# Kernel optimization log

Hardware: AMD Instinct MI355X
Metric: run time of the kernel (lower is better)

Reference implementation:

```python
import jax, jax.numpy as jnp
import numpy as np

N, E, IN, H, C, ED = 50000, 800000, 128, 4, 64, 4
NEG_SLOPE = 0.2


def setup_inputs() -> dict:
    key = jax.random.key(0)
    ks = iter(jax.random.split(key, 40))
    def p(shape, s=0.05):
        return jax.random.normal(next(ks), shape, jnp.float32) * s
    inp = dict(
        x=jax.random.normal(next(ks), (N, IN), jnp.float32),
        edge_index=jax.random.randint(next(ks), (2, E), 0, N),
        edge_attr=jax.random.normal(next(ks), (E, ED), jnp.float32),
        # GATConv layer 1 (concat=True)
        W1=p((IN, H * C)), att_src1=p((H, C)), att_dst1=p((H, C)),
        We1=p((ED, H * C)), att_e1=p((H, C)), b1=p((H * C,)),
        g1=jnp.ones((H * C,), jnp.float32), be1=jnp.zeros((H * C,), jnp.float32),
        # GATConv layer 2 (concat=False -> mean over heads)
        W2=p((H * C, H * C)), att_src2=p((H, C)), att_dst2=p((H, C)),
        We2=p((ED, H * C)), att_e2=p((H, C)), b2=p((C,)),
        g2=jnp.ones((C,), jnp.float32), be2=jnp.zeros((C,), jnp.float32),
        # skip / MLP head
        skip_W=p((IN, C)), skip_b=p((C,)),
        fc1_W=p((C, C // 2)), fc1_b=p((C // 2,)),
        fc2_W=p((C // 2, 1)), fc2_b=p((1,)),
    )
    return inp


def _add_self_loops(edge_index, edge_attr, n):
    # PyG GATConv default: add_self_loops=True, fill_value='mean'
    src, dst = edge_index[0], edge_index[1]
    sums = jax.ops.segment_sum(edge_attr, dst, num_segments=n)
    cnt = jax.ops.segment_sum(jnp.ones((edge_attr.shape[0], 1), edge_attr.dtype), dst, num_segments=n)
    mean_attr = sums / jnp.maximum(cnt, 1.0)
    loop = jnp.arange(n)
    src = jnp.concatenate([src, loop])
    dst = jnp.concatenate([dst, loop])
    ea = jnp.concatenate([edge_attr, mean_attr], axis=0)
    return src, dst, ea


def _gat_layer(x, src, dst, ea, W, a_src, a_dst, We, a_e, bias, n, concat):
    xs = (x @ W).reshape(n, H, C)                     # [N,H,C]
    alpha_src = (xs * a_src).sum(-1)                  # [N,H]
    alpha_dst = (xs * a_dst).sum(-1)                  # [N,H]
    ep = (ea @ We).reshape(-1, H, C)                  # [Et,H,C]
    alpha_e = (ep * a_e).sum(-1)                      # [Et,H]
    alpha = jax.nn.leaky_relu(alpha_src[src] + alpha_dst[dst] + alpha_e, NEG_SLOPE)
    # segment softmax over destination nodes
    m = jax.ops.segment_max(alpha, dst, num_segments=n)
    alpha = jnp.exp(alpha - m[dst])
    denom = jax.ops.segment_sum(alpha, dst, num_segments=n)
    alpha = alpha / (denom[dst] + 1e-16)
    out = jax.ops.segment_sum(xs[src] * alpha[:, :, None], dst, num_segments=n)  # [N,H,C]
    out = out.reshape(n, H * C) if concat else out.mean(axis=1)
    return out + bias


def _bn(x, g, b):
    mu = x.mean(0)
    var = x.var(0)
    return (x - mu) * jax.lax.rsqrt(var + 1e-5) * g + b


def reference(x, edge_index, edge_attr, W1, att_src1, att_dst1, We1, att_e1, b1, g1, be1,
              W2, att_src2, att_dst2, We2, att_e2, b2, g2, be2,
              skip_W, skip_b, fc1_W, fc1_b, fc2_W, fc2_b):
    n = x.shape[0]
    src, dst, ea = _add_self_loops(edge_index, edge_attr, n)
    residual = x @ skip_W + skip_b
    h = _gat_layer(x, src, dst, ea, W1, att_src1, att_dst1, We1, att_e1, b1, n, True)
    h = jax.nn.elu(_bn(h, g1, be1))
    h = _gat_layer(h, src, dst, ea, W2, att_src2, att_dst2, We2, att_e2, b2, n, False)
    h = jax.nn.elu(_bn(h, g2, be2))
    h = h + residual
    h = jax.nn.relu(h @ fc1_W + fc1_b)
    h = jax.nn.softplus(h @ fc2_W + fc2_b)
    return h.squeeze(-1)
```

## Files before the change

### kernel.cpp

```cpp
#include <hip/hip_runtime.h>
#include <math.h>

static constexpr int N_NODES = 50000;
static constexpr int N_EDGES = 800000;
static constexpr int IN_F = 128;
static constexpr int CH = 64;
static constexpr int HC = 256;
static constexpr float NEG_SLOPE = 0.2f;

typedef __attribute__((ext_vector_type(8))) short bf16x8;
typedef __attribute__((ext_vector_type(4))) float f32x4;

__device__ __forceinline__ unsigned pack_bf(float a, float b) {
    unsigned ua = __float_as_uint(a) + 0x8000u;
    unsigned ub = __float_as_uint(b) + 0x8000u;
    return __builtin_amdgcn_perm(ub, ua, 0x07060302u);
}
__device__ __forceinline__ float bflo(unsigned u) { return __uint_as_float(u << 16); }
__device__ __forceinline__ float bfhi(unsigned u) { return __uint_as_float(u & 0xffff0000u); }
__device__ __forceinline__ float bfs(unsigned short u) {
    return __uint_as_float((unsigned)u << 16);
}
__device__ __forceinline__ float elu(float v) { return v > 0.f ? v : __expf(v) - 1.0f; }

__device__ __forceinline__ int sigma(int p) { return ((p & 15) << 4) | (p >> 4); }

static constexpr int EB_BLK = (N_EDGES + 255) / 256;
static constexpr int CONV_ITEMS = 106496 + 32;
static constexpr int CONV_BLK = (CONV_ITEMS + 255) / 256;

__global__ void hist_conv(const int* __restrict__ ei, int* __restrict__ deg,
                          const float* __restrict__ W1, const float* __restrict__ W2,
                          const float* __restrict__ Ws, const float* __restrict__ We1,
                          const float* __restrict__ atte1, const float* __restrict__ We2,
                          const float* __restrict__ atte2, unsigned short* __restrict__ WT1,
                          unsigned short* __restrict__ WT2, unsigned short* __restrict__ WTs,
                          float* __restrict__ weff) {
    if (blockIdx.x < EB_BLK) {
        int e = blockIdx.x * 256 + threadIdx.x;
        if (e < N_EDGES) atomicAdd(&deg[ei[N_EDGES + e]], 1);
        return;
    }
    int t = (blockIdx.x - EB_BLK) * 256 + threadIdx.x;
    if (t < 32768) {
        int k = t >> 8, n = t & 255;
        unsigned u = __float_as_uint(W1[t]) + 0x8000u;
        WT1[n * 128 + k] = (unsigned short)(u >> 16);
    } else if (t < 98304) {
        int u2 = t - 32768;
        int k = u2 >> 8, n = u2 & 255;
        unsigned u = __float_as_uint(W2[u2]) + 0x8000u;
        WT2[n * 256 + sigma(k)] = (unsigned short)(u >> 16);
    } else if (t < 106496) {
        int u2 = t - 98304;
        int k = u2 >> 6, n = u2 & 63;
        unsigned u = __float_as_uint(Ws[u2]) + 0x8000u;
        WTs[n * 128 + k] = (unsigned short)(u >> 16);
    } else if (t < 106496 + 32) {
        int idx = t - 106496;
        const float* We = idx < 16 ? We1 : We2;
        const float* ae = idx < 16 ? atte1 : atte2;
        int j = idx & 15;
        int d = j >> 2, h = j & 3;
        float s = 0.f;
        for (int c = 0; c < CH; ++c) s += We[d * HC + h * CH + c] * ae[h * CH + c];
        weff[idx] = s;
    }
}

__global__ void scan_block(const int* __restrict__ deg, int* __restrict__ rowptr,
                           int* __restrict__ bsum) {
    __shared__ int s[256];
    int tid = threadIdx.x;
    int i = blockIdx.x * 256 + tid;
    int v = (i < N_NODES) ? deg[i] : 0;
    s[tid] = v;
    __syncthreads();
    for (int off = 1; off < 256; off <<= 1) {
        int t = (tid >= off) ? s[tid - off] : 0;
        __syncthreads();
        s[tid] += t;
        __syncthreads();
    }
    if (i < N_NODES) rowptr[i] = s[tid] - v;
    if (tid == 255) bsum[blockIdx.x] = s[255];
}

__global__ void scan_add2(int* __restrict__ rowptr, const int* __restrict__ bsum,
                          int* __restrict__ fillc, int nb) {
    __shared__ int s[256];
    int tid = threadIdx.x;
    int v = (tid < nb) ? bsum[tid] : 0;
    s[tid] = v;
    __syncthreads();
    for (int off = 1; off < 256; off <<= 1) {
        int t = (tid >= off) ? s[tid - off] : 0;
        __syncthreads();
        s[tid] += t;
        __syncthreads();
    }
    int boff = (blockIdx.x == 0) ? 0 : s[blockIdx.x - 1];
    int i = blockIdx.x * 256 + tid;
    if (i < N_NODES) {
        rowptr[i] += boff;
        fillc[i] = 0;
    }
    if (i == N_NODES) rowptr[N_NODES] = N_EDGES;
}

__global__ void csr_fill(const int* __restrict__ ei, const int* __restrict__ rowptr,
                         int* __restrict__ fillc, int* __restrict__ csr_src,
                         int* __restrict__ pos) {
    int e = blockIdx.x * blockDim.x + threadIdx.x;
    if (e >= N_EDGES) return;
    int s = ei[e];
    int t = ei[N_EDGES + e];
    int p = atomicAdd(&fillc[t], 1);
    int i = rowptr[t] + p;
    csr_src[i] = s;
    pos[e] = i;
}

template <int K, bool ABF, bool BN, bool SKIP>
__global__ __launch_bounds__(256) void gemm_mfma_att(
    const void* __restrict__ Av, const unsigned short* __restrict__ BT,
    const float* __restrict__ colsum, const float* __restrict__ g,
    const float* __restrict__ be, float invM,
    const unsigned short* __restrict__ BTs, const float* __restrict__ skip_b,
    float* __restrict__ residual,
    const float* __restrict__ att_src, const float* __restrict__ att_dst,
    unsigned short* __restrict__ xsb, float* __restrict__ asrc, float* __restrict__ adst,
    int M) {
    constexpr int RT = 2, NT = 16;
    __shared__ float s_scale[256], s_shift[256];
    if constexpr (BN) {
        int c = threadIdx.x;
        int tc = sigma(c);
        float mean = colsum[c] * invM;
        float var = colsum[256 + c] * invM - mean * mean;
        float sc = g[tc] * rsqrtf(var + 1e-5f);
        s_scale[c] = sc;
        s_shift[c] = be[tc] - mean * sc;
        __syncthreads();
    }
    const int lane = threadIdx.x & 63;
    const int wid = threadIdx.x >> 6;
    const int r0 = blockIdx.x * (4 * RT * 16) + wid * RT * 16;
    const int lr = lane & 15;
    const int kg = lane >> 4;
    f32x4 acc[RT][NT] = {};
    f32x4 accS[RT][4] = {};
    const float* af = (const float*)Av;
    const unsigned short* ab = (const unsigned short*)Av;
    size_t rowoff[RT];
#pragma unroll
    for (int m = 0; m < RT; ++m) {
        int r = r0 + m * 16 + lr;
        if (r >= M) r = M - 1;
        rowoff[m] = (size_t)r * K + kg * 8;
    }
    const unsigned short* brow = BT + (size_t)lr * K + kg * 8;
    const unsigned short* brow_s = SKIP ? BTs + (size_t)lr * K + kg * 8 : nullptr;
    for (int k0 = 0; k0 < K; k0 += 32) {
        float4 sc0, sc1, sh0, sh1;
        if constexpr (BN) {
            sc0 = *reinterpret_cast<const float4*>(&s_scale[k0 + kg * 8]);
            sc1 = *reinterpret_cast<const float4*>(&s_scale[k0 + kg * 8 + 4]);
            sh0 = *reinterpret_cast<const float4*>(&s_shift[k0 + kg * 8]);
            sh1 = *reinterpret_cast<const float4*>(&s_shift[k0 + kg * 8 + 4]);
        }
        bf16x8 a[RT];
#pragma unroll
        for (int m = 0; m < RT; ++m) {
            if constexpr (!ABF) {
                const float4 lo = *reinterpret_cast<const float4*>(af + rowoff[m] + k0);
                const float4 hi = *reinterpret_cast<const float4*>(af + rowoff[m] + k0 + 4);
                union { bf16x8 v; unsigned u[4]; } fa;
                fa.u[0] = pack_bf(lo.x, lo.y);
                fa.u[1] = pack_bf(lo.z, lo.w);
                fa.u[2] = pack_bf(hi.x, hi.y);
                fa.u[3] = pack_bf(hi.z, hi.w);
                a[m] = fa.v;
            } else {
                union { bf16x8 v; unsigned short us[8]; unsigned u[4]; } fa;
                fa.v = *reinterpret_cast<const bf16x8*>(ab + rowoff[m] + k0);
                if constexpr (BN) {
                    float f0 = elu(fmaf(bfs(fa.us[0]), sc0.x, sh0.x));
                    float f1 = elu(fmaf(bfs(fa.us[1]), sc0.y, sh0.y));
                    float f2 = elu(fmaf(bfs(fa.us[2]), sc0.z, sh0.z));
                    float f3 = elu(fmaf(bfs(fa.us[3]), sc0.w, sh0.w));
                    float f4 = elu(fmaf(bfs(fa.us[4]), sc1.x, sh1.x));
                    float f5 = elu(fmaf(bfs(fa.us[5]), sc1.y, sh1.y));
                    float f6 = elu(fmaf(bfs(fa.us[6]), sc1.z, sh1.z));
                    float f7 = elu(fmaf(bfs(fa.us[7]), sc1.w, sh1.w));
                    fa.u[0] = pack_bf(f0, f1);
                    fa.u[1] = pack_bf(f2, f3);
                    fa.u[2] = pack_bf(f4, f5);
                    fa.u[3] = pack_bf(f6, f7);
                }
                a[m] = fa.v;
            }
        }
#pragma unroll
        for (int c = 0; c < NT; ++c) {
            bf16x8 b = *reinterpret_cast<const bf16x8*>(brow + (size_t)c * 16 * K + k0);
#pragma unroll
            for (int m = 0; m < RT; ++m)
                acc[m][c] = __builtin_amdgcn_mfma_f32_16x16x32_bf16(a[m], b, acc[m][c], 0, 0, 0);
        }
        if constexpr (SKIP) {
#pragma unroll
            for (int c = 0; c < 4; ++c) {
                bf16x8 b = *reinterpret_cast<const bf16x8*>(brow_s + (size_t)c * 16 * K + k0);
#pragma unroll
                for (int m = 0; m < RT; ++m)
                    accS[m][c] =
                        __builtin_amdgcn_mfma_f32_16x16x32_bf16(a[m], b, accS[m][c], 0, 0, 0);
            }
        }
    }
    float attS[NT], attD[NT];
#pragma unroll
    for (int c = 0; c < NT; ++c) {
        attS[c] = att_src[c * 16 + lr];
        attD[c] = att_dst[c * 16 + lr];
    }
#pragma unroll
    for (int m = 0; m < RT; ++m) {
#pragma unroll
        for (int j = 0; j < 4; ++j) {
            int row = r0 + m * 16 + kg * 4 + j;
            bool valid = row < M;
            uint4 ua, ub;
            ua.x = pack_bf(acc[m][0][j], acc[m][1][j]);
            ua.y = pack_bf(acc[m][2][j], acc[m][3][j]);
            ua.z = pack_bf(acc[m][4][j], acc[m][5][j]);
            ua.w = pack_bf(acc[m][6][j], acc[m][7][j]);
            ub.x = pack_bf(acc[m][8][j], acc[m][9][j]);
            ub.y = pack_bf(acc[m][10][j], acc[m][11][j]);
            ub.z = pack_bf(acc[m][12][j], acc[m][13][j]);
            ub.w = pack_bf(acc[m][14][j], acc[m][15][j]);
            if (valid) {
                uint4* dst = reinterpret_cast<uint4*>(xsb + (size_t)row * HC) + lr * 2;
                dst[0] = ua;
                dst[1] = ub;
            }
            if constexpr (SKIP) {
                if (valid) {
#pragma unroll
                    for (int c = 0; c < 4; ++c) {
                        int col = c * 16 + lr;
                        residual[(size_t)row * CH + col] = accS[m][c][j] + skip_b[col];
                    }
                }
            }
#pragma unroll
            for (int h = 0; h < 4; ++h) {
                float ps = acc[m][4 * h + 0][j] * attS[4 * h + 0] +
                           acc[m][4 * h + 1][j] * attS[4 * h + 1] +
                           acc[m][4 * h + 2][j] * attS[4 * h + 2] +
                           acc[m][4 * h + 3][j] * attS[4 * h + 3];
                float pd = acc[m][4 * h + 0][j] * attD[4 * h + 0] +
                           acc[m][4 * h + 1][j] * attD[4 * h + 1] +
                           acc[m][4 * h + 2][j] * attD[4 * h + 2] +
                           acc[m][4 * h + 3][j] * attD[4 * h + 3];
#pragma unroll
                for (int mk = 1; mk < 16; mk <<= 1) {
                    ps += __shfl_xor(ps, mk);
                    pd += __shfl_xor(pd, mk);
                }
                if (valid && lr == 0) {
                    asrc[row * 4 + h] = ps;
                    adst[row * 4 + h] = pd;
                }
            }
        }
    }
}

__global__ __launch_bounds__(256) void edge_w(
    const int* __restrict__ ei, const float4* __restrict__ ea, const int* __restrict__ pos,
    const float* __restrict__ weff, const float4* __restrict__ asrcv,
    const float4* __restrict__ adstv, uint4* __restrict__ pw) {
    int e = blockIdx.x * blockDim.x + threadIdx.x;
    if (e >= N_EDGES) return;
    int s = ei[e];
    int t = ei[N_EDGES + e];
    const float4 v = ea[e];
    const float4 as4 = asrcv[s];
    const float4 ad4 = adstv[t];
    const float asl[4] = {as4.x, as4.y, as4.z, as4.w};
    const float adl[4] = {ad4.x, ad4.y, ad4.z, ad4.w};
    float p[4], aev[4];
#pragma unroll
    for (int h = 0; h < 4; ++h) {
        float ae = v.x * weff[h] + v.y * weff[4 + h] + v.z * weff[8 + h] + v.w * weff[12 + h];
        float l = asl[h] + adl[h] + ae;
        l = fmaxf(l, NEG_SLOPE * l);
        p[h] = __expf(l);
        aev[h] = ae;
    }
    pw[pos[e]] = make_uint4(pack_bf(p[0], p[1]), pack_bf(p[2], p[3]),
                            pack_bf(aev[0], aev[1]), pack_bf(aev[2], aev[3]));
}

template <bool MEAN>
__global__ __launch_bounds__(256) void gat_node(
    const int* __restrict__ rowptr, const int* __restrict__ csr_src,
    const uint4* __restrict__ pw, const float4* __restrict__ asrcv,
    const float4* __restrict__ adstv, const uint2* __restrict__ xsb,
    float* __restrict__ zbuf, void* __restrict__ outp) {
    if (blockIdx.x == 0) {
        zbuf[threadIdx.x] = 0.f;
        zbuf[256 + threadIdx.x] = 0.f;
    }
    int t = blockIdx.x * 4 + (threadIdx.x >> 6);
    if (t >= N_NODES) return;
    const int lane = threadIdx.x & 63;
    const int h = lane & 3;
    const unsigned sh = (h & 1) ? 0u : 16u;
    const bool hiW = (h & 2) != 0;
    const int start = rowptr[t], end = rowptr[t + 1];
    const int deg = end - start;
    const uint2* xl = xsb + lane;
    float acc0 = 0.f, acc1 = 0.f, acc2 = 0.f, acc3 = 0.f;
    float psum = 0.f, aesum = 0.f;
    int i = start;
    for (; i + 8 <= end; i += 8) {
        uint2 f[8];
        float p[8], ae[8];
#pragma unroll
        for (int j = 0; j < 8; ++j) {
            int s = csr_src[i + j];
            f[j] = xl[(size_t)s * 64];
            const uint4 w = pw[i + j];
            unsigned pword = hiW ? w.y : w.x;
            unsigned aeword = hiW ? w.w : w.z;
            p[j] = __uint_as_float((pword << sh) & 0xffff0000u);
            ae[j] = __uint_as_float((aeword << sh) & 0xffff0000u);
        }
#pragma unroll
        for (int j = 0; j < 8; ++j) {
            psum += p[j];
            aesum += ae[j];
            acc0 += bflo(f[j].x) * p[j];
            acc1 += bfhi(f[j].x) * p[j];
            acc2 += bflo(f[j].y) * p[j];
            acc3 += bfhi(f[j].y) * p[j];
        }
    }
    for (; i < end; ++i) {
        int s = csr_src[i];
        uint2 f = xl[(size_t)s * 64];
        const uint4 w = pw[i];
        unsigned pword = hiW ? w.y : w.x;
        unsigned aeword = hiW ? w.w : w.z;
        float p = __uint_as_float((pword << sh) & 0xffff0000u);
        float ae = __uint_as_float((aeword << sh) & 0xffff0000u);
        psum += p;
        aesum += ae;
        acc0 += bflo(f.x) * p;
        acc1 += bfhi(f.x) * p;
        acc2 += bflo(f.y) * p;
        acc3 += bfhi(f.y) * p;
    }
    const float inv_deg = deg > 0 ? 1.0f / (float)deg : 1.0f;
    const float4 as4 = asrcv[t];
    const float4 ad4 = adstv[t];
    float asl = h == 0 ? as4.x : h == 1 ? as4.y : h == 2 ? as4.z : as4.w;
    float adl = h == 0 ? ad4.x : h == 1 ? ad4.y : h == 2 ? ad4.z : ad4.w;
    float l = asl + adl + aesum * inv_deg;
    l = fmaxf(l, NEG_SLOPE * l);
    const float pself = __expf(l);
    uint2 sf = xl[(size_t)t * 64];
    acc0 += bflo(sf.x) * pself;
    acc1 += bfhi(sf.x) * pself;
    acc2 += bflo(sf.y) * pself;
    acc3 += bfhi(sf.y) * pself;
    const float inv = 1.0f / (psum + pself + 1e-16f);
    acc0 *= inv; acc1 *= inv; acc2 *= inv; acc3 *= inv;
    if constexpr (MEAN) {
        acc0 += __shfl_xor(acc0, 1); acc0 += __shfl_xor(acc0, 2);
        acc1 += __shfl_xor(acc1, 1); acc1 += __shfl_xor(acc1, 2);
        acc2 += __shfl_xor(acc2, 1); acc2 += __shfl_xor(acc2, 2);
        acc3 += __shfl_xor(acc3, 1); acc3 += __shfl_xor(acc3, 2);
        if (h == 0) {
            int q = lane >> 2;
            float* o = reinterpret_cast<float*>(outp) + (size_t)t * CH + q;
            o[0] = 0.25f * acc0;
            o[16] = 0.25f * acc1;
            o[32] = 0.25f * acc2;
            o[48] = 0.25f * acc3;
        }
    } else {
        reinterpret_cast<uint2*>(outp)[(size_t)t * 64 + lane] =
            make_uint2(pack_bf(acc0, acc1), pack_bf(acc2, acc3));
    }
}

__global__ void colstats_bf(const unsigned short* __restrict__ X, float* __restrict__ sum,
                            float* __restrict__ sumsq, int M) {
    int c = threadIdx.x;
    int r0 = blockIdx.x * 256;
    int r1 = min(M, r0 + 256);
    float s = 0.f, q = 0.f;
    for (int r = r0; r < r1; ++r) {
        float v = bfs(X[(size_t)r * HC + c]);
        s += v;
        q += v * v;
    }
    atomicAdd(&sum[c], s);
    atomicAdd(&sumsq[c], q);
}

template <int F>
__global__ void colstats(const float* __restrict__ X, float* __restrict__ sum,
                         float* __restrict__ sumsq, int M) {
    const int NG = 256 / F;
    int c = threadIdx.x % F;
    int g = threadIdx.x / F;
    int r0 = blockIdx.x * 256;
    int r1 = min(M, r0 + 256);
    float s = 0.f, q = 0.f;
    for (int r = r0 + g; r < r1; r += NG) {
        float v = X[(size_t)r * F + c];
        s += v;
        q += v * v;
    }
    atomicAdd(&sum[c], s);
    atomicAdd(&sumsq[c], q);
}

__global__ __launch_bounds__(256) void head_mlp(
    const float* __restrict__ h2, const float* __restrict__ colsum,
    const float* __restrict__ g2, const float* __restrict__ be2, float invM,
    const float* __restrict__ residual, const float* __restrict__ fc1W,
    const float* __restrict__ fc1b, const float* __restrict__ fc2W,
    const float* __restrict__ fc2b, float* __restrict__ out) {
    __shared__ float s_sc[CH], s_sh[CH];
    if (threadIdx.x < CH) {
        int c = threadIdx.x;
        float mean = colsum[c] * invM;
        float var = colsum[256 + c] * invM - mean * mean;
        float sc = g2[c] * rsqrtf(var + 1e-5f);
        s_sc[c] = sc;
        s_sh[c] = be2[c] - mean * sc;
    }
    __syncthreads();
    int n = blockIdx.x * 4 + (threadIdx.x >> 6);
    if (n >= N_NODES) return;
    int w = threadIdx.x >> 6;
    int lane = threadIdx.x & 63;
    __shared__ float hrow[4][64];
    float v = fmaf(h2[(size_t)n * CH + lane], s_sc[lane], s_sh[lane]);
    v = elu(v) + residual[(size_t)n * CH + lane];
    hrow[w][lane] = v;
    float p = 0.f;
    if (lane < 32) {
        float acc = fc1b[lane];
#pragma unroll
        for (int k = 0; k < CH; ++k) acc = fmaf(hrow[w][k], fc1W[k * 32 + lane], acc);
        acc = fmaxf(acc, 0.f);
        p = acc * fc2W[lane];
    }
    for (int off = 16; off > 0; off >>= 1) p += __shfl_down(p, off);
    if (lane == 0) {
        float z = p + fc2b[0];
        out[n] = z > 20.f ? z : log1pf(expf(z));
    }
}

extern "C" void kernel_launch(void* const* d_in, const int* in_sizes, int n_in, void* d_out,
                              int out_size, void* d_ws, size_t ws_size, hipStream_t stream) {
    const float* x        = (const float*)d_in[0];
    const int*   ei       = (const int*)d_in[1];
    const float* ea       = (const float*)d_in[2];
    const float* W1       = (const float*)d_in[3];
    const float* att_src1 = (const float*)d_in[4];
    const float* att_dst1 = (const float*)d_in[5];
    const float* We1      = (const float*)d_in[6];
    const float* att_e1   = (const float*)d_in[7];
    const float* g1       = (const float*)d_in[9];
    const float* be1      = (const float*)d_in[10];
    const float* W2       = (const float*)d_in[11];
    const float* att_src2 = (const float*)d_in[12];
    const float* att_dst2 = (const float*)d_in[13];
    const float* We2      = (const float*)d_in[14];
    const float* att_e2   = (const float*)d_in[15];
    const float* g2       = (const float*)d_in[17];
    const float* be2      = (const float*)d_in[18];
    const float* skip_W   = (const float*)d_in[19];
    const float* skip_b   = (const float*)d_in[20];
    const float* fc1_W    = (const float*)d_in[21];
    const float* fc1_b    = (const float*)d_in[22];
    const float* fc2_W    = (const float*)d_in[23];
    const float* fc2_b    = (const float*)d_in[24];
    float* out = (float*)d_out;

    float* wsf = (float*)d_ws;
    size_t off = 0;
    auto take = [&](size_t n) {
        float* p = wsf + off;
        off += n;
        return p;
    };
    unsigned short* xsb  = (unsigned short*)take((size_t)N_NODES * HC / 2);
    unsigned short* aggb = (unsigned short*)take((size_t)N_NODES * HC / 2);
    uint4* pw       = (uint4*)take((size_t)N_EDGES * 4);
    int* csr_src    = (int*)take(N_EDGES);
    int* pos        = (int*)take(N_EDGES);
    int* rowptr     = (int*)take(N_NODES + 1);
    int* degfill    = (int*)take(N_NODES);
    int* bsum       = (int*)take(256);
    float* asrc     = take(N_NODES * 4);
    float* adst     = take(N_NODES * 4);
    float* residual = take((size_t)N_NODES * CH);
    float* h2       = take((size_t)N_NODES * CH);
    float* weff     = take(32);
    float* colsum   = take(HC);
    float* colsq    = take(HC);
    unsigned short* WT1 = (unsigned short*)take(IN_F * HC / 2);
    unsigned short* WT2 = (unsigned short*)take(HC * HC / 2);
    unsigned short* WTs = (unsigned short*)take(IN_F * CH / 2);

    const int NBLK = (N_NODES + 255) / 256;
    const int NODE4 = (N_NODES + 3) / 4;
    const float invM = 1.0f / N_NODES;

    hipMemsetAsync(degfill, 0, N_NODES * sizeof(int), stream);
    hist_conv<<<EB_BLK + CONV_BLK, 256, 0, stream>>>(ei, degfill, W1, W2, skip_W, We1,
                                                     att_e1, We2, att_e2, WT1, WT2, WTs, weff);
    scan_block<<<NBLK, 256, 0, stream>>>(degfill, rowptr, bsum);
    scan_add2<<<(N_NODES + 256) / 256, 256, 0, stream>>>(rowptr, bsum, degfill, NBLK);
    csr_fill<<<EB_BLK, 256, 0, stream>>>(ei, rowptr, degfill, csr_src, pos);

    gemm_mfma_att<IN_F, false, false, true><<<(N_NODES + 127) / 128, 256, 0, stream>>>(
        x, WT1, nullptr, nullptr, nullptr, 0.f, WTs, skip_b, residual, att_src1, att_dst1,
        xsb, asrc, adst, N_NODES);
    edge_w<<<EB_BLK, 256, 0, stream>>>(ei, (const float4*)ea, pos, weff, (const float4*)asrc,
                                       (const float4*)adst, pw);
    gat_node<false><<<NODE4, 256, 0, stream>>>(rowptr, csr_src, pw, (const float4*)asrc,
                                               (const float4*)adst, (const uint2*)xsb,
                                               colsum, aggb);
    colstats_bf<<<NBLK, 256, 0, stream>>>(aggb, colsum, colsq, N_NODES);

    gemm_mfma_att<HC, true, true, false><<<(N_NODES + 127) / 128, 256, 0, stream>>>(
        aggb, WT2, colsum, g1, be1, invM, nullptr, nullptr, nullptr, att_src2, att_dst2,
        xsb, asrc, adst, N_NODES);
    edge_w<<<EB_BLK, 256, 0, stream>>>(ei, (const float4*)ea, pos, weff + 16,
                                       (const float4*)asrc, (const float4*)adst, pw);
    gat_node<true><<<NODE4, 256, 0, stream>>>(rowptr, csr_src, pw, (const float4*)asrc,
                                              (const float4*)adst, (const uint2*)xsb,
                                              colsum, h2);
    colstats<CH><<<NBLK, 256, 0, stream>>>(h2, colsum, colsq, N_NODES);

    head_mlp<<<NODE4, 256, 0, stream>>>(h2, colsum, g2, be2, invM, residual, fc1_W, fc1_b,
                                        fc2_W, fc2_b, out);
}
```

Baseline: 508.1 us.

## Fuse CSR fill into first GEMM launch and permute edge data to CSR order

The csr_fill kernel is folded into the first GEMM launch as extra blocks, which removes one launch and lets the fill overlap with the GEMM. The fill now also writes csr_dst and an edge_attr array permuted into CSR order. edge_w can then read contiguously and write pw[i] directly instead of scattering through pos. The GEMM row tile is also halved from 32 to 16 rows per wave, giving more blocks and fewer registers per thread but less B-operand reuse. The cost is an extra 12.8MB permuted edge buffer written once.

```diff
diff --git a/kernel.cpp b/kernel.cpp
--- a/kernel.cpp
+++ b/kernel.cpp
@@ -28,6 +28,7 @@
 static constexpr int EB_BLK = (N_EDGES + 255) / 256;
 static constexpr int CONV_ITEMS = 106496 + 32;
 static constexpr int CONV_BLK = (CONV_ITEMS + 255) / 256;
+static constexpr int GEMM_BLKS = (N_NODES + 63) / 64;
 
 __global__ void hist_conv(const int* __restrict__ ei, int* __restrict__ deg,
                           const float* __restrict__ W1, const float* __restrict__ W2,
@@ -108,20 +109,7 @@
     if (i == N_NODES) rowptr[N_NODES] = N_EDGES;
 }
 
-__global__ void csr_fill(const int* __restrict__ ei, const int* __restrict__ rowptr,
-                         int* __restrict__ fillc, int* __restrict__ csr_src,
-                         int* __restrict__ pos) {
-    int e = blockIdx.x * blockDim.x + threadIdx.x;
-    if (e >= N_EDGES) return;
-    int s = ei[e];
-    int t = ei[N_EDGES + e];
-    int p = atomicAdd(&fillc[t], 1);
-    int i = rowptr[t] + p;
-    csr_src[i] = s;
-    pos[e] = i;
-}
-
-template <int K, bool ABF, bool BN, bool SKIP>
+template <int K, bool ABF, bool BN, bool SKIP, bool FILL>
 __global__ __launch_bounds__(256) void gemm_mfma_att(
     const void* __restrict__ Av, const unsigned short* __restrict__ BT,
     const float* __restrict__ colsum, const float* __restrict__ g,
@@ -130,8 +118,25 @@
     float* __restrict__ residual,
     const float* __restrict__ att_src, const float* __restrict__ att_dst,
     unsigned short* __restrict__ xsb, float* __restrict__ asrc, float* __restrict__ adst,
-    int M) {
-    constexpr int RT = 2, NT = 16;
+    int M, const int* __restrict__ ei, const float4* __restrict__ ea,
+    const int* __restrict__ rowptr, int* __restrict__ fillc, int* __restrict__ csr_src,
+    int* __restrict__ csr_dst, float4* __restrict__ eaperm) {
+    if constexpr (FILL) {
+        if (blockIdx.x >= GEMM_BLKS) {
+            int e = (blockIdx.x - GEMM_BLKS) * 256 + threadIdx.x;
+            if (e < N_EDGES) {
+                int s = ei[e];
+                int t = ei[N_EDGES + e];
+                int p = atomicAdd(&fillc[t], 1);
+                int i = rowptr[t] + p;
+                csr_src[i] = s;
+                csr_dst[i] = t;
+                eaperm[i] = ea[e];
+            }
+            return;
+        }
+    }
+    constexpr int NT = 16;
     __shared__ float s_scale[256], s_shift[256];
     if constexpr (BN) {
         int c = threadIdx.x;
@@ -145,20 +150,16 @@
     }
     const int lane = threadIdx.x & 63;
     const int wid = threadIdx.x >> 6;
-    const int r0 = blockIdx.x * (4 * RT * 16) + wid * RT * 16;
+    const int r0 = blockIdx.x * 64 + wid * 16;
     const int lr = lane & 15;
     const int kg = lane >> 4;
-    f32x4 acc[RT][NT] = {};
-    f32x4 accS[RT][4] = {};
+    f32x4 acc[NT] = {};
+    f32x4 accS[4] = {};
     const float* af = (const float*)Av;
     const unsigned short* ab = (const unsigned short*)Av;
-    size_t rowoff[RT];
-#pragma unroll
-    for (int m = 0; m < RT; ++m) {
-        int r = r0 + m * 16 + lr;
-        if (r >= M) r = M - 1;
-        rowoff[m] = (size_t)r * K + kg * 8;
-    }
+    int rr = r0 + lr;
+    if (rr >= M) rr = M - 1;
+    const size_t rowoff = (size_t)rr * K + kg * 8;
     const unsigned short* brow = BT + (size_t)lr * K + kg * 8;
     const unsigned short* brow_s = SKIP ? BTs + (size_t)lr * K + kg * 8 : nullptr;
     for (int k0 = 0; k0 < K; k0 += 32) {
@@ -169,53 +170,45 @@
             sh0 = *reinterpret_cast<const float4*>(&s_shift[k0 + kg * 8]);
             sh1 = *reinterpret_cast<const float4*>(&s_shift[k0 + kg * 8 + 4]);
         }
-        bf16x8 a[RT];
-#pragma unroll
-        for (int m = 0; m < RT; ++m) {
-            if constexpr (!ABF) {
-                const float4 lo = *reinterpret_cast<const float4*>(af + rowoff[m] + k0);
-                const float4 hi = *reinterpret_cast<const float4*>(af + rowoff[m] + k0 + 4);
-                union { bf16x8 v; unsigned u[4]; } fa;
-                fa.u[0] = pack_bf(lo.x, lo.y);
-                fa.u[1] = pack_bf(lo.z, lo.w);
-                fa.u[2] = pack_bf(hi.x, hi.y);
-                fa.u[3] = pack_bf(hi.z, hi.w);
-                a[m] = fa.v;
-            } else {
-                union { bf16x8 v; unsigned short us[8]; unsigned u[4]; } fa;
-                fa.v = *reinterpret_cast<const bf16x8*>(ab + rowoff[m] + k0);
-                if constexpr (BN) {
-                    float f0 = elu(fmaf(bfs(fa.us[0]), sc0.x, sh0.x));
-                    float f1 = elu(fmaf(bfs(fa.us[1]), sc0.y, sh0.y));
-                    float f2 = elu(fmaf(bfs(fa.us[2]), sc0.z, sh0.z));
-                    float f3 = elu(fmaf(bfs(fa.us[3]), sc0.w, sh0.w));
-                    float f4 = elu(fmaf(bfs(fa.us[4]), sc1.x, sh1.x));
-                    float f5 = elu(fmaf(bfs(fa.us[5]), sc1.y, sh1.y));
-                    float f6 = elu(fmaf(bfs(fa.us[6]), sc1.z, sh1.z));
-                    float f7 = elu(fmaf(bfs(fa.us[7]), sc1.w, sh1.w));
-                    fa.u[0] = pack_bf(f0, f1);
-                    fa.u[1] = pack_bf(f2, f3);
-                    fa.u[2] = pack_bf(f4, f5);
-                    fa.u[3] = pack_bf(f6, f7);
-                }
-                a[m] = fa.v;
+        bf16x8 a;
+        if constexpr (!ABF) {
+            const float4 lo = *reinterpret_cast<const float4*>(af + rowoff + k0);
+            const float4 hi = *reinterpret_cast<const float4*>(af + rowoff + k0 + 4);
+            union { bf16x8 v; unsigned u[4]; } fa;
+            fa.u[0] = pack_bf(lo.x, lo.y);
+            fa.u[1] = pack_bf(lo.z, lo.w);
+            fa.u[2] = pack_bf(hi.x, hi.y);
+            fa.u[3] = pack_bf(hi.z, hi.w);
+            a = fa.v;
+        } else {
+            union { bf16x8 v; unsigned short us[8]; unsigned u[4]; } fa;
+            fa.v = *reinterpret_cast<const bf16x8*>(ab + rowoff + k0);
+            if constexpr (BN) {
+                float f0 = elu(fmaf(bfs(fa.us[0]), sc0.x, sh0.x));
+                float f1 = elu(fmaf(bfs(fa.us[1]), sc0.y, sh0.y));
+                float f2 = elu(fmaf(bfs(fa.us[2]), sc0.z, sh0.z));
+                float f3 = elu(fmaf(bfs(fa.us[3]), sc0.w, sh0.w));
+                float f4 = elu(fmaf(bfs(fa.us[4]), sc1.x, sh1.x));
+                float f5 = elu(fmaf(bfs(fa.us[5]), sc1.y, sh1.y));
+                float f6 = elu(fmaf(bfs(fa.us[6]), sc1.z, sh1.z));
+                float f7 = elu(fmaf(bfs(fa.us[7]), sc1.w, sh1.w));
+                fa.u[0] = pack_bf(f0, f1);
+                fa.u[1] = pack_bf(f2, f3);
+                fa.u[2] = pack_bf(f4, f5);
+                fa.u[3] = pack_bf(f6, f7);
             }
+            a = fa.v;
         }
 #pragma unroll
         for (int c = 0; c < NT; ++c) {
             bf16x8 b = *reinterpret_cast<const bf16x8*>(brow + (size_t)c * 16 * K + k0);
-#pragma unroll
-            for (int m = 0; m < RT; ++m)
-                acc[m][c] = __builtin_amdgcn_mfma_f32_16x16x32_bf16(a[m], b, acc[m][c], 0, 0, 0);
+            acc[c] = __builtin_amdgcn_mfma_f32_16x16x32_bf16(a, b, acc[c], 0, 0, 0);
         }
         if constexpr (SKIP) {
 #pragma unroll
             for (int c = 0; c < 4; ++c) {
                 bf16x8 b = *reinterpret_cast<const bf16x8*>(brow_s + (size_t)c * 16 * K + k0);
-#pragma unroll
-                for (int m = 0; m < RT; ++m)
-                    accS[m][c] =
-                        __builtin_amdgcn_mfma_f32_16x16x32_bf16(a[m], b, accS[m][c], 0, 0, 0);
+                accS[c] = __builtin_amdgcn_mfma_f32_16x16x32_bf16(a, b, accS[c], 0, 0, 0);
             }
         }
     }
@@ -226,67 +219,65 @@
         attD[c] = att_dst[c * 16 + lr];
     }
 #pragma unroll
-    for (int m = 0; m < RT; ++m) {
-#pragma unroll
-        for (int j = 0; j < 4; ++j) {
-            int row = r0 + m * 16 + kg * 4 + j;
-            bool valid = row < M;
-            uint4 ua, ub;
-            ua.x = pack_bf(acc[m][0][j], acc[m][1][j]);
-            ua.y = pack_bf(acc[m][2][j], acc[m][3][j]);
-            ua.z = pack_bf(acc[m][4][j], acc[m][5][j]);
-            ua.w = pack_bf(acc[m][6][j], acc[m][7][j]);
-            ub.x = pack_bf(acc[m][8][j], acc[m][9][j]);
-            ub.y = pack_bf(acc[m][10][j], acc[m][11][j]);
-            ub.z = pack_bf(acc[m][12][j], acc[m][13][j]);
-            ub.w = pack_bf(acc[m][14][j], acc[m][15][j]);
+    for (int j = 0; j < 4; ++j) {
+        int row = r0 + kg * 4 + j;
+        bool valid = row < M;
+        uint4 ua, ub;
+        ua.x = pack_bf(acc[0][j], acc[1][j]);
+        ua.y = pack_bf(acc[2][j], acc[3][j]);
+        ua.z = pack_bf(acc[4][j], acc[5][j]);
+        ua.w = pack_bf(acc[6][j], acc[7][j]);
+        ub.x = pack_bf(acc[8][j], acc[9][j]);
+        ub.y = pack_bf(acc[10][j], acc[11][j]);
+        ub.z = pack_bf(acc[12][j], acc[13][j]);
+        ub.w = pack_bf(acc[14][j], acc[15][j]);
+        if (valid) {
+            uint4* dst = reinterpret_cast<uint4*>(xsb + (size_t)row * HC) + lr * 2;
+            dst[0] = ua;
+            dst[1] = ub;
+        }
+        if constexpr (SKIP) {
             if (valid) {
-                uint4* dst = reinterpret_cast<uint4*>(xsb + (size_t)row * HC) + lr * 2;
-                dst[0] = ua;
-                dst[1] = ub;
-            }
-            if constexpr (SKIP) {
-                if (valid) {
-#pragma unroll
-                    for (int c = 0; c < 4; ++c) {
-                        int col = c * 16 + lr;
-                        residual[(size_t)row * CH + col] = accS[m][c][j] + skip_b[col];
-                    }
+#pragma unroll
+                for (int c = 0; c < 4; ++c) {
+                    int col = c * 16 + lr;
+                    residual[(size_t)row * CH + col] = accS[c][j] + skip_b[col];
                 }
             }
-#pragma unroll
-            for (int h = 0; h < 4; ++h) {
-                float ps = acc[m][4 * h + 0][j] * attS[4 * h + 0] +
-                           acc[m][4 * h + 1][j] * attS[4 * h + 1] +
-                           acc[m][4 * h + 2][j] * attS[4 * h + 2] +
-                           acc[m][4 * h + 3][j] * attS[4 * h + 3];
-                float pd = acc[m][4 * h + 0][j] * attD[4 * h + 0] +
-                           acc[m][4 * h + 1][j] * attD[4 * h + 1] +
-                           acc[m][4 * h + 2][j] * attD[4 * h + 2] +
-                           acc[m][4 * h + 3][j] * attD[4 * h + 3];
-#pragma unroll
-                for (int mk = 1; mk < 16; mk <<= 1) {
-                    ps += __shfl_xor(ps, mk);
-                    pd += __shfl_xor(pd, mk);
-                }
-                if (valid && lr == 0) {
-                    asrc[row * 4 + h] = ps;
-                    adst[row * 4 + h] = pd;
-                }
+        }
+#pragma unroll
+        for (int h = 0; h < 4; ++h) {
+            float ps = acc[4 * h + 0][j] * attS[4 * h + 0] +
+                       acc[4 * h + 1][j] * attS[4 * h + 1] +
+                       acc[4 * h + 2][j] * attS[4 * h + 2] +
+                       acc[4 * h + 3][j] * attS[4 * h + 3];
+            float pd = acc[4 * h + 0][j] * attD[4 * h + 0] +
+                       acc[4 * h + 1][j] * attD[4 * h + 1] +
+                       acc[4 * h + 2][j] * attD[4 * h + 2] +
+                       acc[4 * h + 3][j] * attD[4 * h + 3];
+#pragma unroll
+            for (int mk = 1; mk < 16; mk <<= 1) {
+                ps += __shfl_xor(ps, mk);
+                pd += __shfl_xor(pd, mk);
             }
+            if (valid && lr == 0) {
+                asrc[row * 4 + h] = ps;
+                adst[row * 4 + h] = pd;
+            }
         }
     }
 }
 
 __global__ __launch_bounds__(256) void edge_w(
-    const int* __restrict__ ei, const float4* __restrict__ ea, const int* __restrict__ pos,
-    const float* __restrict__ weff, const float4* __restrict__ asrcv,
-    const float4* __restrict__ adstv, uint4* __restrict__ pw) {
-    int e = blockIdx.x * blockDim.x + threadIdx.x;
-    if (e >= N_EDGES) return;
-    int s = ei[e];
-    int t = ei[N_EDGES + e];
-    const float4 v = ea[e];
+    const int* __restrict__ csr_src, const int* __restrict__ csr_dst,
+    const float4* __restrict__ eaperm, const float* __restrict__ weff,
+    const float4* __restrict__ asrcv, const float4* __restrict__ adstv,
+    uint4* __restrict__ pw) {
+    int i = blockIdx.x * 256 + threadIdx.x;
+    if (i >= N_EDGES) return;
+    int s = csr_src[i];
+    int t = csr_dst[i];
+    const float4 v = eaperm[i];
     const float4 as4 = asrcv[s];
     const float4 ad4 = adstv[t];
     const float asl[4] = {as4.x, as4.y, as4.z, as4.w};
@@ -300,8 +291,8 @@
         p[h] = __expf(l);
         aev[h] = ae;
     }
-    pw[pos[e]] = make_uint4(pack_bf(p[0], p[1]), pack_bf(p[2], p[3]),
-                            pack_bf(aev[0], aev[1]), pack_bf(aev[2], aev[3]));
+    pw[i] = make_uint4(pack_bf(p[0], p[1]), pack_bf(p[2], p[3]),
+                       pack_bf(aev[0], aev[1]), pack_bf(aev[2], aev[3]));
 }
 
 template <bool MEAN>
@@ -507,8 +498,9 @@
     unsigned short* xsb  = (unsigned short*)take((size_t)N_NODES * HC / 2);
     unsigned short* aggb = (unsigned short*)take((size_t)N_NODES * HC / 2);
     uint4* pw       = (uint4*)take((size_t)N_EDGES * 4);
+    float4* eaperm  = (float4*)take((size_t)N_EDGES * 4);
     int* csr_src    = (int*)take(N_EDGES);
-    int* pos        = (int*)take(N_EDGES);
+    int* csr_dst    = (int*)take(N_EDGES);
     int* rowptr     = (int*)take(N_NODES + 1);
     int* degfill    = (int*)take(N_NODES);
     int* bsum       = (int*)take(256);
@@ -532,22 +524,24 @@
                                                      att_e1, We2, att_e2, WT1, WT2, WTs, weff);
     scan_block<<<NBLK, 256, 0, stream>>>(degfill, rowptr, bsum);
     scan_add2<<<(N_NODES + 256) / 256, 256, 0, stream>>>(rowptr, bsum, degfill, NBLK);
-    csr_fill<<<EB_BLK, 256, 0, stream>>>(ei, rowptr, degfill, csr_src, pos);
-
-    gemm_mfma_att<IN_F, false, false, true><<<(N_NODES + 127) / 128, 256, 0, stream>>>(
-        x, WT1, nullptr, nullptr, nullptr, 0.f, WTs, skip_b, residual, att_src1, att_dst1,
-        xsb, asrc, adst, N_NODES);
-    edge_w<<<EB_BLK, 256, 0, stream>>>(ei, (const float4*)ea, pos, weff, (const float4*)asrc,
+
+    gemm_mfma_att<IN_F, false, false, true, true>
+        <<<GEMM_BLKS + EB_BLK, 256, 0, stream>>>(
+            x, WT1, nullptr, nullptr, nullptr, 0.f, WTs, skip_b, residual, att_src1,
+            att_dst1, xsb, asrc, adst, N_NODES, ei, (const float4*)ea, rowptr, degfill,
+            csr_src, csr_dst, eaperm);
+    edge_w<<<EB_BLK, 256, 0, stream>>>(csr_src, csr_dst, eaperm, weff, (const float4*)asrc,
                                        (const float4*)adst, pw);
     gat_node<false><<<NODE4, 256, 0, stream>>>(rowptr, csr_src, pw, (const float4*)asrc,
                                                (const float4*)adst, (const uint2*)xsb,
                                                colsum, aggb);
     colstats_bf<<<NBLK, 256, 0, stream>>>(aggb, colsum, colsq, N_NODES);
 
-    gemm_mfma_att<HC, true, true, false><<<(N_NODES + 127) / 128, 256, 0, stream>>>(
+    gemm_mfma_att<HC, true, true, false, false><<<GEMM_BLKS, 256, 0, stream>>>(
         aggb, WT2, colsum, g1, be1, invM, nullptr, nullptr, nullptr, att_src2, att_dst2,
-        xsb, asrc, adst, N_NODES);
-    edge_w<<<EB_BLK, 256, 0, stream>>>(ei, (const float4*)ea, pos, weff + 16,
+        xsb, asrc, adst, N_NODES, nullptr, nullptr, nullptr, nullptr, nullptr, nullptr,
+        nullptr);
+    edge_w<<<EB_BLK, 256, 0, stream>>>(csr_src, csr_dst, eaperm, weff + 16,
                                        (const float4*)asrc, (const float4*)adst, pw);
     gat_node<true><<<NODE4, 256, 0, stream>>>(rowptr, csr_src, pw, (const float4*)asrc,
                                               (const float4*)adst, (const uint2*)xsb,
```

After: 497.1 us. 2.2% less time.
